# Kernel tuning notes

Measured on AMD Instinct MI355X. Metric: run time of the kernel, lower is better.

## Reference

```python
import jax, jax.numpy as jnp
import numpy as np

B, S = 32, 256          # sequences, tokens per sequence (prefill)
DIM, NH, NKV, HD = 2048, 16, 16, 128
CLS, GRID, BASE = 1, 16, 10000


def precompute_freqs_cis_2d(grid_size, n_elem, base, cls_token_num):
    half = n_elem // 2
    freqs = 1.0 / (base ** (np.arange(0, half, 2)[: half // 2].astype(np.float32) / half))
    t = np.arange(grid_size, dtype=np.float32)
    fr = np.outer(t, freqs)                      # [grid, half//2]
    fg = np.concatenate([
        np.broadcast_to(fr[:, None, :], (grid_size, grid_size, fr.shape[1])),
        np.broadcast_to(fr[None, :, :], (grid_size, grid_size, fr.shape[1])),
    ], axis=-1)                                  # [grid, grid, half]
    cache = np.stack([np.cos(fg), np.sin(fg)], axis=-1).reshape(grid_size * grid_size, half, 2)
    cond = np.concatenate([np.zeros((cls_token_num, half, 2), np.float32), cache.astype(np.float32)], axis=0)
    return jnp.asarray(cond)                     # [cls+grid^2, half, 2]

FREQS = precompute_freqs_cis_2d(GRID, HD, BASE, CLS)


def _apply_rope(x, fc):
    # x: [T, H, HD], fc: [T, HD//2, 2]
    xr = x.reshape(x.shape[0], x.shape[1], HD // 2, 2)
    c = fc[:, None, :, 0]
    s = fc[:, None, :, 1]
    out = jnp.stack([xr[..., 0] * c - xr[..., 1] * s,
                     xr[..., 1] * c + xr[..., 0] * s], axis=-1)
    return out.reshape(x.shape)


def setup_inputs() -> dict:
    key = jax.random.key(0)
    k1, k2, k3 = jax.random.split(key, 3)
    x = jax.random.normal(k1, (B * S, DIM), dtype=jnp.float32)
    positions = jnp.tile(jnp.arange(S, dtype=jnp.int32), B)  # per-seq positions 0..S-1
    total_kv = (NH + 2 * NKV) * HD
    wqkv = jax.random.normal(k2, (total_kv, DIM), dtype=jnp.float32) * 0.02
    wo = jax.random.normal(k3, (DIM, DIM), dtype=jnp.float32) * 0.02
    return {"x": x, "positions": positions, "wqkv": wqkv, "wo": wo}


def reference(x, positions, wqkv, wo):
    T = x.shape[0]
    kv_size = NKV * HD
    qkv = x @ wqkv.T                               # [T, dim + 2*kv_size]
    xq, xk, xv = jnp.split(qkv, [DIM, DIM + kv_size], axis=-1)
    q = xq.reshape(T, NH, HD)
    k = xk.reshape(T, NKV, HD)
    v = xv.reshape(T, NKV, HD)

    fc = FREQS[positions]                          # [T, HD//2, 2]
    q = _apply_rope(q, fc)
    k = _apply_rope(k, fc)

    # paged attention (prefill): causal attention within each sequence
    qb = q.reshape(B, S, NH, HD)
    kb = k.reshape(B, S, NKV, HD)
    vb = v.reshape(B, S, NKV, HD)
    scale = HD ** -0.5
    scores = jnp.einsum("bqhd,bkhd->bhqk", qb, kb) * scale   # [B,H,S,S]
    causal = jnp.tril(jnp.ones((S, S), dtype=bool))
    scores = jnp.where(causal[None, None], scores, jnp.finfo(scores.dtype).min)
    attn = jax.nn.softmax(scores, axis=-1)
    out = jnp.einsum("bhqk,bkhd->bqhd", attn, vb).reshape(T, DIM)
    return out @ wo.T
```

## Files before the change

kernel.cpp:

```cpp
#include <hip/hip_runtime.h>
#include <cstddef>


typedef float    f32x4 __attribute__((ext_vector_type(4)));
typedef _Float16 f16x8 __attribute__((ext_vector_type(8)));
typedef _Float16 f16x4 __attribute__((ext_vector_type(4)));

#define LOG2E 1.4426950408889634f
#define NLOG2B_32 (-0.41524101186192697f)

__device__ static inline f32x4 mfma16x32(f16x8 a, f16x8 b, f32x4 c) {
  return __builtin_amdgcn_mfma_f32_16x16x32_f16(a, b, c, 0, 0, 0);
}

__device__ static inline void gload16(const void* g, void* lds) {
  __builtin_amdgcn_global_load_lds(
      (const __attribute__((address_space(1))) unsigned int*)g,
      (__attribute__((address_space(3))) unsigned int*)lds, 16, 0, 0);
}

#define BAR()    asm volatile("s_barrier" ::: "memory")
#define VMCNT6() asm volatile("s_waitcnt vmcnt(6)" ::: "memory")

__global__ void cvt3_f32_f16(const float* __restrict__ s0, _Float16* __restrict__ d0,
                             const float* __restrict__ s1, _Float16* __restrict__ d1,
                             const float* __restrict__ s2, _Float16* __restrict__ d2) {
  int i = blockIdx.x * blockDim.x + threadIdx.x;
  const float* src; _Float16* dst;
  if (i < 4194304)      { src = s0; dst = d0; }
  else if (i < 7340032) { src = s1; dst = d1; i -= 4194304; }
  else                  { src = s2; dst = d2; i -= 7340032; }
  f32x4 v = *(const f32x4*)(src + (size_t)i * 4);
  f16x4 o;
  o[0] = (_Float16)v[0]; o[1] = (_Float16)v[1];
  o[2] = (_Float16)v[2]; o[3] = (_Float16)v[3];
  *(f16x4*)(dst + (size_t)i * 4) = o;
}

template <typename OutT>
__global__ void __launch_bounds__(512, 2)
gemm_bt5(const _Float16* __restrict__ A, const _Float16* __restrict__ Bt,
         OutT* __restrict__ C, int M, int N, int K) {
  __shared__ __attribute__((aligned(16))) _Float16 Ab[2][256 * 64];
  __shared__ __attribute__((aligned(16))) _Float16 Bb[2][256 * 64];

  const int tid  = threadIdx.x;
  const int lane = tid & 63;
  const int w    = tid >> 6;
  const int wm   = w >> 2, wn = w & 3;
  const int g    = lane >> 4, li = lane & 15;

  const int nwg = (int)gridDim.x;
  const int cpx = nwg >> 3;
  const int bid = (int)blockIdx.x;
  const int swz = (bid & 7) * cpx + (bid >> 3);
  const int nbn = N >> 8;
  const int bm  = (swz / nbn) << 8;
  const int bn  = (swz % nbn) << 8;
  const int NT  = K >> 6;

  const int srow = tid >> 3;
  const int scol = ((tid & 7) ^ (srow & 7)) * 8;
  const _Float16* gA = A  + (size_t)(bm + srow) * K + scol;
  const _Float16* gB = Bt + (size_t)(bn + srow) * K + scol;
  const int sdst = w * 1024;

  auto stage = [&](const _Float16* gbase, _Float16* lbase, int h, int kt) {
    const _Float16* gp = gbase + (size_t)h * 128 * K + kt;
    char* lp = (char*)lbase + h * 16384;
#pragma unroll
    for (int j = 0; j < 2; ++j)
      gload16(gp + (size_t)j * 64 * K, lp + j * 8192 + sdst);
  };

  auto rdfrag = [&](const _Float16* buf, int row, int k2) -> f16x8 {
    const int pc = ((k2 << 2) + g) ^ (li & 7);
    return *(const f16x8*)((const char*)buf + row * 128 + pc * 16);
  };

  f32x4 acc[8][4] = {};

  stage(gA, Ab[0], 0, 0);
  stage(gB, Bb[0], 0, 0);
  stage(gB, Bb[0], 1, 0);
  stage(gA, Ab[0], 1, 0);
  stage(gA, Ab[1], 0, (NT > 1) ? 64 : 0);
  VMCNT6();
  BAR();

  for (int T = 0; T < NT; ++T) {
    const int cb = T & 1, nb = cb ^ 1;
    const _Float16* Ac = Ab[cb];
    const _Float16* Bc = Bb[cb];
    const int ktN  = (T + 1 < NT) ? (T + 1) << 6 : 0;
    const int ktN2 = (T + 2 < NT) ? (T + 2) << 6 : 0;

    f16x8 af0[4][2], af1[4][2], bf0[2][2], bf1[2][2];

#pragma unroll
    for (int m = 0; m < 4; ++m)
#pragma unroll
      for (int k2 = 0; k2 < 2; ++k2)
        af0[m][k2] = rdfrag(Ac, wm * 128 + m * 16 + li, k2);
#pragma unroll
    for (int n = 0; n < 2; ++n)
#pragma unroll
      for (int k2 = 0; k2 < 2; ++k2)
        bf0[n][k2] = rdfrag(Bc, wn * 64 + n * 16 + li, k2);
    stage(gB, Bb[nb], 0, ktN);
    __builtin_amdgcn_s_setprio(1);
#pragma unroll
    for (int m = 0; m < 4; ++m)
#pragma unroll
      for (int n = 0; n < 2; ++n)
#pragma unroll
        for (int k2 = 0; k2 < 2; ++k2)
          acc[m][n] = mfma16x32(af0[m][k2], bf0[n][k2], acc[m][n]);
    __builtin_amdgcn_s_setprio(0);
    VMCNT6();
    BAR();

#pragma unroll
    for (int n = 0; n < 2; ++n)
#pragma unroll
      for (int k2 = 0; k2 < 2; ++k2)
        bf1[n][k2] = rdfrag(Bc, wn * 64 + (n + 2) * 16 + li, k2);
    stage(gB, Bb[nb], 1, ktN);
    __builtin_amdgcn_s_setprio(1);
#pragma unroll
    for (int m = 0; m < 4; ++m)
#pragma unroll
      for (int n = 0; n < 2; ++n)
#pragma unroll
        for (int k2 = 0; k2 < 2; ++k2)
          acc[m][n + 2] = mfma16x32(af0[m][k2], bf1[n][k2], acc[m][n + 2]);
    __builtin_amdgcn_s_setprio(0);
    VMCNT6();
    BAR();

#pragma unroll
    for (int m = 0; m < 4; ++m)
#pragma unroll
      for (int k2 = 0; k2 < 2; ++k2)
        af1[m][k2] = rdfrag(Ac, wm * 128 + (m + 4) * 16 + li, k2);
    stage(gA, Ab[nb], 1, ktN);
    __builtin_amdgcn_s_setprio(1);
#pragma unroll
    for (int m = 0; m < 4; ++m)
#pragma unroll
      for (int n = 0; n < 2; ++n)
#pragma unroll
        for (int k2 = 0; k2 < 2; ++k2)
          acc[m + 4][n] = mfma16x32(af1[m][k2], bf0[n][k2], acc[m + 4][n]);
    __builtin_amdgcn_s_setprio(0);
    VMCNT6();
    BAR();

    stage(gA, Ab[cb], 0, ktN2);
    __builtin_amdgcn_s_setprio(1);
#pragma unroll
    for (int m = 0; m < 4; ++m)
#pragma unroll
      for (int n = 0; n < 2; ++n)
#pragma unroll
        for (int k2 = 0; k2 < 2; ++k2)
          acc[m + 4][n + 2] = mfma16x32(af1[m][k2], bf1[n][k2], acc[m + 4][n + 2]);
    __builtin_amdgcn_s_setprio(0);
    VMCNT6();
    BAR();
  }

  asm volatile("s_waitcnt vmcnt(0)" ::: "memory");

#pragma unroll
  for (int m = 0; m < 8; ++m)
#pragma unroll
    for (int n = 0; n < 4; ++n)
#pragma unroll
      for (int r = 0; r < 4; ++r) {
        const int row = bm + wm * 128 + m * 16 + g * 4 + r;
        const int col = bn + wn * 64 + n * 16 + li;
        C[(size_t)row * N + col] = (OutT)acc[m][n][r];
      }
}

__global__ void rope_kernel(_Float16* __restrict__ qkv,
                            const int* __restrict__ positions) {
  const int idx = blockIdx.x * blockDim.x + threadIdx.x;
  const int ch = idx & 15;
  const int hh = (idx >> 4) & 31;
  const int t  = idx >> 9;
  _Float16* p = qkv + (size_t)t * 6144 + hh * 128 + ch * 8;
  const int pos = positions[t];
  f16x8 v = *(const f16x8*)p;
  f16x8 o;
  if (pos == 0) {
#pragma unroll
    for (int u = 0; u < 8; ++u) o[u] = (_Float16)0.f;
  } else {
    const int gi = pos - 1;
    const float tv = (ch < 8) ? (float)(gi >> 4) : (float)(gi & 15);
#pragma unroll
    for (int u = 0; u < 4; ++u) {
      const int k2 = (ch * 4 + u) & 31;
      const float freq = exp2f((float)k2 * NLOG2B_32);
      const float ang = tv * freq;
      float s, c;
      sincosf(ang, &s, &c);
      const float x0 = (float)v[2 * u];
      const float x1 = (float)v[2 * u + 1];
      o[2 * u]     = (_Float16)(x0 * c - x1 * s);
      o[2 * u + 1] = (_Float16)(x1 * c + x0 * s);
    }
  }
  *(f16x8*)p = o;
}

__global__ void __launch_bounds__(512)
attn_kernel(const _Float16* __restrict__ qkv, _Float16* __restrict__ O) {
  const int b  = blockIdx.x >> 4;
  const int h  = blockIdx.x & 15;
  const int tb = b << 8;
  const int tid = threadIdx.x;
  const int lane = tid & 63;
  const int w = tid >> 6;
  const int g = lane >> 4, li = lane & 15;

  __shared__ __attribute__((aligned(16))) _Float16 Ks[64 * 128];
  __shared__ __attribute__((aligned(16))) _Float16 Vt[128 * 64];
  __shared__ __attribute__((aligned(16))) _Float16 Ps[8][32 * 40];

  const int qb[2]   = {w, 15 - w};
  const int qrow[2] = {qb[0] * 16, qb[1] * 16};
  const int kmax[2] = {qb[0] >> 2, qb[1] >> 2};

  f16x8 qf[2][4];
#pragma unroll
  for (int rb = 0; rb < 2; ++rb)
#pragma unroll
    for (int ks = 0; ks < 4; ++ks)
      qf[rb][ks] = *(const f16x8*)(qkv + (size_t)(tb + qrow[rb] + li) * 6144
                                   + h * 128 + ks * 32 + g * 8);

  f32x4 oacc[2][8] = {};
  float m_r[2][4], l_r[2][4];
#pragma unroll
  for (int rb = 0; rb < 2; ++rb)
#pragma unroll
    for (int r = 0; r < 4; ++r) { m_r[rb][r] = -1e30f; l_r[rb][r] = 0.f; }

  const float scale = 0.08838834764831845f;

  for (int kt = 0; kt < 4; ++kt) {
#pragma unroll
    for (int i = 0; i < 2; ++i) {
      const int s = i * 512 + tid;
      const int key = s >> 4;
      const int sch = (s & 15) ^ (key & 7);
      const _Float16* gk = qkv + (size_t)(tb + kt * 64 + key) * 6144
                           + 2048 + h * 128 + sch * 8;
      gload16(gk, (char*)Ks + (i * 512 + (tid & ~63)) * 16);
    }
#pragma unroll
    for (int i = 0; i < 2; ++i) {
      const int s = i * 512 + tid;
      const int key = s >> 4;
      const int chv = s & 15;
      f16x8 v = *(const f16x8*)(qkv + (size_t)(tb + kt * 64 + key) * 6144
                                + 4096 + h * 128 + chv * 8);
#pragma unroll
      for (int e = 0; e < 8; ++e) {
        const int d = chv * 8 + e;
        const int blk = ((key >> 3) ^ (d & 7) ^ ((d >> 3) & 7)) & 7;
        Vt[d * 64 + blk * 8 + (key & 7)] = v[e];
      }
    }
    __syncthreads();

    const bool act[2] = {kt <= kmax[0], kt <= kmax[1]};
    if (act[0] || act[1]) {
      f32x4 sacc[2][4] = {};
#pragma unroll
      for (int ks = 0; ks < 4; ++ks) {
        f16x8 kf[4];
#pragma unroll
        for (int cb = 0; cb < 4; ++cb) {
          const int key = cb * 16 + li;
          const int chunk = (ks * 4 + g) ^ (key & 7);
          kf[cb] = *(const f16x8*)((const char*)Ks + key * 256 + chunk * 16);
        }
#pragma unroll
        for (int rb = 0; rb < 2; ++rb)
          if (act[rb])
#pragma unroll
            for (int cb = 0; cb < 4; ++cb)
              sacc[rb][cb] = mfma16x32(qf[rb][ks], kf[cb], sacc[rb][cb]);
      }
#pragma unroll
      for (int rb = 0; rb < 2; ++rb) {
        if (!act[rb]) continue;
#pragma unroll
        for (int r = 0; r < 4; ++r) {
          const int q = qrow[rb] + g * 4 + r;
          float mx = -1e30f;
#pragma unroll
          for (int cb = 0; cb < 4; ++cb) {
            float sv = sacc[rb][cb][r] * scale;
            const int key = kt * 64 + cb * 16 + li;
            sv = (key <= q) ? sv : -1e30f;
            sacc[rb][cb][r] = sv;
            mx = fmaxf(mx, sv);
          }
#pragma unroll
          for (int off = 1; off < 16; off <<= 1)
            mx = fmaxf(mx, __shfl_xor(mx, off));
          const float mold = m_r[rb][r];
          const float mnew = fmaxf(mold, mx);
          const float alpha = exp2f((mold - mnew) * LOG2E);
          float rsum = 0.f;
#pragma unroll
          for (int cb = 0; cb < 4; ++cb) {
            const float pv = exp2f((sacc[rb][cb][r] - mnew) * LOG2E);
            sacc[rb][cb][r] = pv;
            rsum += pv;
          }
#pragma unroll
          for (int off = 1; off < 16; off <<= 1)
            rsum += __shfl_xor(rsum, off);
          m_r[rb][r] = mnew;
          l_r[rb][r] = l_r[rb][r] * alpha + rsum;
#pragma unroll
          for (int db = 0; db < 8; ++db)
            oacc[rb][db][r] *= alpha;
        }
      }
#pragma unroll
      for (int ks2 = 0; ks2 < 2; ++ks2) {
#pragma unroll
        for (int rb = 0; rb < 2; ++rb) {
          if (!act[rb]) continue;
#pragma unroll
          for (int cbh = 0; cbh < 2; ++cbh) {
            const int cb = ks2 * 2 + cbh;
#pragma unroll
            for (int r = 0; r < 4; ++r)
              Ps[w][(rb * 16 + g * 4 + r) * 40 + cbh * 16 + li] =
                  (_Float16)sacc[rb][cb][r];
          }
        }
        asm volatile("s_waitcnt lgkmcnt(0)" ::: "memory");
        f16x8 pa[2];
#pragma unroll
        for (int rb = 0; rb < 2; ++rb)
          if (act[rb])
            pa[rb] = *(const f16x8*)(&Ps[w][(rb * 16 + li) * 40 + g * 8]);
#pragma unroll
        for (int db = 0; db < 8; ++db) {
          const int d = db * 16 + li;
          const int keych = ks2 * 4 + g;
          const int blk = (keych ^ (d & 7) ^ ((d >> 3) & 7)) & 7;
          const f16x8 vf = *(const f16x8*)(&Vt[d * 64 + blk * 8]);
#pragma unroll
          for (int rb = 0; rb < 2; ++rb)
            if (act[rb])
              oacc[rb][db] = mfma16x32(pa[rb], vf, oacc[rb][db]);
        }
      }
    }
    __syncthreads();
  }
#pragma unroll
  for (int rb = 0; rb < 2; ++rb)
#pragma unroll
    for (int db = 0; db < 8; ++db)
#pragma unroll
      for (int r = 0; r < 4; ++r) {
        const int row = tb + qrow[rb] + g * 4 + r;
        const int col = h * 128 + db * 16 + li;
        O[(size_t)row * 2048 + col] = (_Float16)(oacc[rb][db][r] / l_r[rb][r]);
      }
}

extern "C" void kernel_launch(void* const* d_in, const int* in_sizes, int n_in,
                              void* d_out, int out_size, void* d_ws, size_t ws_size,
                              hipStream_t stream) {
  const float* x         = (const float*)d_in[0];
  const int*   positions = (const int*)d_in[1];
  const float* wqkv      = (const float*)d_in[2];
  const float* wo        = (const float*)d_in[3];
  float* out = (float*)d_out;

  char* ws = (char*)d_ws;
  _Float16* qkv    = (_Float16*)(ws);
  _Float16* xf     = (_Float16*)(ws + 100663296);
  _Float16* wqkvf  = (_Float16*)(ws + 134217728);
  _Float16* wof    = (_Float16*)(ws + 159383552);
  _Float16* of     = xf;

  cvt3_f32_f16<<<32768, 256, 0, stream>>>(x, xf, wqkv, wqkvf, wo, wof);

  gemm_bt5<_Float16><<<768, 512, 0, stream>>>(xf, wqkvf, qkv, 8192, 6144, 2048);

  rope_kernel<<<16384, 256, 0, stream>>>(qkv, positions);

  attn_kernel<<<512, 512, 0, stream>>>(qkv, of);

  gemm_bt5<float><<<256, 512, 0, stream>>>(of, wof, out, 8192, 2048, 2048);
}
```

Before: 367.8 us.

## Fuse RoPE into attention kernel using per-block sin/cos LDS table

```diff
diff --git a/kernel.cpp b/kernel.cpp
--- a/kernel.cpp
+++ b/kernel.cpp
@@ -184,40 +184,9 @@
       }
 }
 
-__global__ void rope_kernel(_Float16* __restrict__ qkv,
-                            const int* __restrict__ positions) {
-  const int idx = blockIdx.x * blockDim.x + threadIdx.x;
-  const int ch = idx & 15;
-  const int hh = (idx >> 4) & 31;
-  const int t  = idx >> 9;
-  _Float16* p = qkv + (size_t)t * 6144 + hh * 128 + ch * 8;
-  const int pos = positions[t];
-  f16x8 v = *(const f16x8*)p;
-  f16x8 o;
-  if (pos == 0) {
-#pragma unroll
-    for (int u = 0; u < 8; ++u) o[u] = (_Float16)0.f;
-  } else {
-    const int gi = pos - 1;
-    const float tv = (ch < 8) ? (float)(gi >> 4) : (float)(gi & 15);
-#pragma unroll
-    for (int u = 0; u < 4; ++u) {
-      const int k2 = (ch * 4 + u) & 31;
-      const float freq = exp2f((float)k2 * NLOG2B_32);
-      const float ang = tv * freq;
-      float s, c;
-      sincosf(ang, &s, &c);
-      const float x0 = (float)v[2 * u];
-      const float x1 = (float)v[2 * u + 1];
-      o[2 * u]     = (_Float16)(x0 * c - x1 * s);
-      o[2 * u + 1] = (_Float16)(x1 * c + x0 * s);
-    }
-  }
-  *(f16x8*)p = o;
-}
-
 __global__ void __launch_bounds__(512)
-attn_kernel(const _Float16* __restrict__ qkv, _Float16* __restrict__ O) {
+attn_kernel(const _Float16* __restrict__ qkv, _Float16* __restrict__ O,
+            const int* __restrict__ positions) {
   const int b  = blockIdx.x >> 4;
   const int h  = blockIdx.x & 15;
   const int tb = b << 8;
@@ -229,6 +198,17 @@
   __shared__ __attribute__((aligned(16))) _Float16 Ks[64 * 128];
   __shared__ __attribute__((aligned(16))) _Float16 Vt[128 * 64];
   __shared__ __attribute__((aligned(16))) _Float16 Ps[8][32 * 40];
+  __shared__ float2 tab[512];
+  __shared__ int    ptab[256];
+
+  {
+    const float ang = (float)(tid >> 5) * exp2f((float)(tid & 31) * NLOG2B_32);
+    float s, c;
+    sincosf(ang, &s, &c);
+    tab[tid] = make_float2(c, s);
+    if (tid < 256) ptab[tid] = positions[tb + tid];
+  }
+  __syncthreads();
 
   const int qb[2]   = {w, 15 - w};
   const int qrow[2] = {qb[0] * 16, qb[1] * 16};
@@ -236,11 +216,30 @@
 
   f16x8 qf[2][4];
 #pragma unroll
-  for (int rb = 0; rb < 2; ++rb)
-#pragma unroll
-    for (int ks = 0; ks < 4; ++ks)
-      qf[rb][ks] = *(const f16x8*)(qkv + (size_t)(tb + qrow[rb] + li) * 6144
-                                   + h * 128 + ks * 32 + g * 8);
+  for (int rb = 0; rb < 2; ++rb) {
+    const int pos = ptab[qrow[rb] + li];
+    const int iv = (pos - 1) >> 4, jv = (pos - 1) & 15;
+#pragma unroll
+    for (int ks = 0; ks < 4; ++ks) {
+      f16x8 v = *(const f16x8*)(qkv + (size_t)(tb + qrow[rb] + li) * 6144
+                                + h * 128 + ks * 32 + g * 8);
+      f16x8 o;
+      if (pos == 0) {
+#pragma unroll
+        for (int u = 0; u < 8; ++u) o[u] = (_Float16)0.f;
+      } else {
+        const int tv = (ks < 2) ? iv : jv;
+#pragma unroll
+        for (int u = 0; u < 4; ++u) {
+          const float2 cs = tab[tv * 32 + ((ks * 16 + g * 4 + u) & 31)];
+          const float x0 = (float)v[2 * u], x1 = (float)v[2 * u + 1];
+          o[2 * u]     = (_Float16)(x0 * cs.x - x1 * cs.y);
+          o[2 * u + 1] = (_Float16)(x1 * cs.x + x0 * cs.y);
+        }
+      }
+      qf[rb][ks] = o;
+    }
+  }
 
   f32x4 oacc[2][8] = {};
   float m_r[2][4], l_r[2][4];
@@ -256,10 +255,26 @@
     for (int i = 0; i < 2; ++i) {
       const int s = i * 512 + tid;
       const int key = s >> 4;
-      const int sch = (s & 15) ^ (key & 7);
-      const _Float16* gk = qkv + (size_t)(tb + kt * 64 + key) * 6144
-                           + 2048 + h * 128 + sch * 8;
-      gload16(gk, (char*)Ks + (i * 512 + (tid & ~63)) * 16);
+      const int c   = s & 15;
+      f16x8 v = *(const f16x8*)(qkv + (size_t)(tb + kt * 64 + key) * 6144
+                                + 2048 + h * 128 + c * 8);
+      const int pos = ptab[kt * 64 + key];
+      f16x8 o;
+      if (pos == 0) {
+#pragma unroll
+        for (int u = 0; u < 8; ++u) o[u] = (_Float16)0.f;
+      } else {
+        const int iv = (pos - 1) >> 4, jv = (pos - 1) & 15;
+        const int tv = (c < 8) ? iv : jv;
+#pragma unroll
+        for (int u = 0; u < 4; ++u) {
+          const float2 cs = tab[tv * 32 + ((c * 4 + u) & 31)];
+          const float x0 = (float)v[2 * u], x1 = (float)v[2 * u + 1];
+          o[2 * u]     = (_Float16)(x0 * cs.x - x1 * cs.y);
+          o[2 * u + 1] = (_Float16)(x1 * cs.x + x0 * cs.y);
+        }
+      }
+      *(f16x8*)((char*)Ks + key * 256 + (c ^ (key & 7)) * 16) = o;
     }
 #pragma unroll
     for (int i = 0; i < 2; ++i) {
@@ -401,9 +416,7 @@
 
   gemm_bt5<_Float16><<<768, 512, 0, stream>>>(xf, wqkvf, qkv, 8192, 6144, 2048);
 
-  rope_kernel<<<16384, 256, 0, stream>>>(qkv, positions);
-
-  attn_kernel<<<512, 512, 0, stream>>>(qkv, of);
+  attn_kernel<<<512, 512, 0, stream>>>(qkv, of, positions);
 
   gemm_bt5<float><<<256, 512, 0, stream>>>(of, wof, out, 8192, 2048, 2048);
 }
```

Result: faster. 346.2 us (-5.9%).
